# Kernel tuning notes

Hardware: AMD Instinct MI355X
Metric: run time of the kernel (lower is better)

The kernel has to match this reference:

```python
import jax, jax.numpy as jnp
import numpy as np

B, N, S, FIN, H, P = 16, 96, 4, 8, 32, 256  # graphs, nodes, edge feats, node feats, channels, pref pairs


def setup_inputs() -> dict:
    key = jax.random.key(0)
    ks = jax.random.split(key, 12)
    xf = jax.random.normal(ks[0], (B, N, FIN), jnp.float32)
    mask = (jax.random.uniform(ks[1], (B, N, 1)) < 0.9).astype(jnp.float32)
    x = jnp.concatenate([xf, mask], axis=-1)  # last column = node mask (GraphMasking)
    a = (jax.random.uniform(ks[2], (B, N, N)) < 0.1).astype(jnp.float32)  # dense binary adjacency
    e = jax.random.normal(ks[3], (B, N, N, S), jnp.float32)
    pref_a = jax.random.randint(ks[4], (P,), 0, B)
    pref_b = jax.random.randint(ks[5], (P,), 0, B)
    g = lambda k, sh: jax.random.normal(k, sh, jnp.float32) * 0.1
    return dict(
        x=x, a=a, e=e, pref_a=pref_a, pref_b=pref_b,
        W1=g(ks[6], (S, FIN * H)), b1=jnp.zeros((FIN * H,), jnp.float32),
        root1=g(ks[7], (FIN, H)), bias1=jnp.zeros((H,), jnp.float32),
        W2=g(ks[8], (S, H * H)), b2=jnp.zeros((H * H,), jnp.float32),
        root2=g(ks[9], (H, H)), bias2=jnp.zeros((H,), jnp.float32),
        Wd=g(ks[10], (H, 1)), bd=jnp.zeros((1,), jnp.float32),
    )


def ecc_conv(x, a, e, W, b, root, bias, mask, fin, fout):
    # Edge-conditioned filter: Dense(S -> fin*fout) per edge, reshaped [B,N,N,fout,fin]
    K = (e @ W + b).reshape(e.shape[0], e.shape[1], e.shape[2], fout, fin)
    # out[b,n,c] = sum_i a[b,n,i] * sum_f K[b,n,i,c,f] * x[b,i,f]
    out = jnp.einsum("bni,bnicf,bif->bnc", a, K, x)
    out = out + x @ root + bias   # root skip + bias
    out = out * mask              # keras mask propagated from GraphMasking
    return jax.nn.relu(out)


def reference(x, a, e, pref_a, pref_b, W1, b1, root1, bias1, W2, b2, root2, bias2, Wd, bd):
    mask = x[..., -1:]            # GraphMasking: strip mask column
    h = x[..., :-1]
    h = ecc_conv(h, a, e, W1, b1, root1, bias1, mask, FIN, H)
    h = ecc_conv(h, a, e, W2, b2, root2, bias2, mask, H, H)
    pooled = jnp.sum(h, axis=1)                 # GlobalSumPool -> [B, H]
    score = jax.nn.relu(pooled @ Wd + bd)       # Dense(1, relu) -> [B, 1]
    return score[pref_a] - score[pref_b]        # pref_lookup diff -> [P, 1]
```

## Files before the change

### kernel.cpp

```cpp
#include <hip/hip_runtime.h>

namespace {
constexpr int NB   = 16;
constexpr int NN   = 96;
constexpr int NS   = 4;
constexpr int NFIN = 8;
constexpr int NH   = 32;
constexpr int NP   = 256;
constexpr int NPB  = 8;
constexpr int NCHUNK = NN / NPB;

__global__ __launch_bounds__(256) void k1_layer1(
    const float* __restrict__ x, const float* __restrict__ a,
    const float* __restrict__ e, const float* __restrict__ W1,
    const float* __restrict__ b1, const float* __restrict__ root1,
    const float* __restrict__ bias1, float* __restrict__ h1out)
{
  const int bb    = blockIdx.y;
  const int chunk = blockIdx.x;
  const int t     = threadIdx.x;
  const int g     = t >> 5;
  const int lane  = t & 31;
  const int gn    = chunk * NPB + g;

  __shared__ float  xf[NN][NFIN];
  __shared__ float  xmask[NN];
  __shared__ int    idxL[NPB][NN];
  __shared__ float  avalL[NPB][NN];
  __shared__ float  aeL[NPB][NN * NS];
  __shared__ float4 T1s[NPB][8];
  __shared__ float4 U1s[NPB][2];

  for (int j = t; j < NN * 9; j += 256) {
    int node = j / 9, ch = j - node * 9;
    float v = x[(bb * NN + node) * 9 + ch];
    if (ch < NFIN) xf[node][ch] = v; else xmask[node] = v;
  }

  const float* arow = a + (size_t)(bb * NN + gn) * NN;
  const float* erow = e + (size_t)(bb * NN + gn) * NN * NS;
  int base = 0;
  for (int r = 0; r < 3; ++r) {
    int i = r * 32 + lane;
    float av = arow[i];
    unsigned long long bal = __ballot(av != 0.0f);
    unsigned int m = ((t & 63) < 32) ? (unsigned int)bal : (unsigned int)(bal >> 32);
    int pref = __popc(m & ((1u << lane) - 1u));
    if (av != 0.0f) {
      int slot = base + pref;
      idxL[g][slot]  = i;
      avalL[g][slot] = av;
      float4 e4 = *(const float4*)(erow + i * NS);
      aeL[g][slot * 4 + 0] = av * e4.x;
      aeL[g][slot * 4 + 1] = av * e4.y;
      aeL[g][slot * 4 + 2] = av * e4.z;
      aeL[g][slot * 4 + 3] = av * e4.w;
    }
    base += __popc(m);
  }
  const int cnt = base;
  __syncthreads();

  const int s = lane >> 3, f = lane & 7;
  float accT = 0.f, accU = 0.f;
  for (int j = 0; j < cnt; ++j) {
    int   idx = idxL[g][j];
    float av  = avalL[g][j];
    float ae  = aeL[g][j * 4 + s];
    float hv  = xf[idx][f];
    accT = fmaf(ae, hv, accT);
    accU = fmaf(av, hv, accU);
  }
  ((float*)T1s[g])[s * 8 + f] = accT;
  if (s == 0) ((float*)U1s[g])[f] = accU;
  __syncthreads();

  const int c = lane;
  float E = bias1[c];
  const float4* W1_4 = (const float4*)W1;
  for (int ss = 0; ss < 4; ++ss)
    for (int f4 = 0; f4 < 2; ++f4) {
      float4 w  = W1_4[ss * 64 + c * 2 + f4];
      float4 tt = T1s[g][ss * 2 + f4];
      E = fmaf(w.x, tt.x, E); E = fmaf(w.y, tt.y, E);
      E = fmaf(w.z, tt.z, E); E = fmaf(w.w, tt.w, E);
    }
  const float4* b1_4 = (const float4*)b1;
  for (int q = 0; q < 2; ++q) {
    float4 w = b1_4[c * 2 + q];
    float4 u = U1s[g][q];
    E = fmaf(w.x, u.x, E); E = fmaf(w.y, u.y, E);
    E = fmaf(w.z, u.z, E); E = fmaf(w.w, u.w, E);
  }
  for (int ff = 0; ff < NFIN; ++ff)
    E = fmaf(xf[gn][ff], root1[ff * NH + c], E);
  float hv = E * xmask[gn];
  h1out[(size_t)(bb * NN + gn) * NH + c] = hv > 0.f ? hv : 0.f;
}

__global__ __launch_bounds__(256) void k2_layer2(
    const float* __restrict__ x, const float* __restrict__ a,
    const float* __restrict__ e, const float* __restrict__ W2,
    const float* __restrict__ b2, const float* __restrict__ root2,
    const float* __restrict__ bias2, const float* __restrict__ h1,
    float* __restrict__ poolp)
{
  const int bb    = blockIdx.y;
  const int chunk = blockIdx.x;
  const int t     = threadIdx.x;
  const int g     = t >> 5;
  const int lane  = t & 31;
  const int gn    = chunk * NPB + g;

  __shared__ float4 h1s[NN * 8];
  __shared__ int    idxL[NPB][NN];
  __shared__ float  avalL[NPB][NN];
  __shared__ float  aeL[NPB][NN * NS];
  __shared__ float4 T2s[NPB][32];
  __shared__ float4 U2s[NPB][8];
  __shared__ float  h2s[NPB][NH];
  __shared__ float  maskL[NPB];

  const float4* h1v = (const float4*)h1;
  for (int j = t; j < NN * 8; j += 256) h1s[j] = h1v[(size_t)bb * NN * 8 + j];
  if (lane == 0) maskL[g] = x[(size_t)(bb * NN + gn) * 9 + 8];

  const float* arow = a + (size_t)(bb * NN + gn) * NN;
  const float* erow = e + (size_t)(bb * NN + gn) * NN * NS;
  int base = 0;
  for (int r = 0; r < 3; ++r) {
    int i = r * 32 + lane;
    float av = arow[i];
    unsigned long long bal = __ballot(av != 0.0f);
    unsigned int m = ((t & 63) < 32) ? (unsigned int)bal : (unsigned int)(bal >> 32);
    int pref = __popc(m & ((1u << lane) - 1u));
    if (av != 0.0f) {
      int slot = base + pref;
      idxL[g][slot]  = i;
      avalL[g][slot] = av;
      float4 e4 = *(const float4*)(erow + i * NS);
      aeL[g][slot * 4 + 0] = av * e4.x;
      aeL[g][slot * 4 + 1] = av * e4.y;
      aeL[g][slot * 4 + 2] = av * e4.z;
      aeL[g][slot * 4 + 3] = av * e4.w;
    }
    base += __popc(m);
  }
  const int cnt = base;
  __syncthreads();

  const int s = lane >> 3, f4 = lane & 7;
  float4 accT = make_float4(0.f, 0.f, 0.f, 0.f);
  float4 accU = make_float4(0.f, 0.f, 0.f, 0.f);
  for (int j = 0; j < cnt; ++j) {
    int    idx = idxL[g][j];
    float  av  = avalL[g][j];
    float  ae  = aeL[g][j * 4 + s];
    float4 h4  = h1s[idx * 8 + f4];
    accT.x = fmaf(ae, h4.x, accT.x); accT.y = fmaf(ae, h4.y, accT.y);
    accT.z = fmaf(ae, h4.z, accT.z); accT.w = fmaf(ae, h4.w, accT.w);
    accU.x = fmaf(av, h4.x, accU.x); accU.y = fmaf(av, h4.y, accU.y);
    accU.z = fmaf(av, h4.z, accU.z); accU.w = fmaf(av, h4.w, accU.w);
  }
  T2s[g][s * 8 + f4] = accT;
  if (s == 0) U2s[g][f4] = accU;
  __syncthreads();

  const int c = lane;
  float E = bias2[c];
  const float4* W2_4 = (const float4*)W2;
  for (int ss = 0; ss < 4; ++ss)
    for (int q = 0; q < 8; ++q) {
      float4 w  = W2_4[ss * 256 + c * 8 + q];
      float4 tt = T2s[g][ss * 8 + q];
      E = fmaf(w.x, tt.x, E); E = fmaf(w.y, tt.y, E);
      E = fmaf(w.z, tt.z, E); E = fmaf(w.w, tt.w, E);
    }
  const float4* b2_4 = (const float4*)b2;
  for (int q = 0; q < 8; ++q) {
    float4 w = b2_4[c * 8 + q];
    float4 u = U2s[g][q];
    E = fmaf(w.x, u.x, E); E = fmaf(w.y, u.y, E);
    E = fmaf(w.z, u.z, E); E = fmaf(w.w, u.w, E);
  }
  for (int q = 0; q < 8; ++q) {
    float4 hh = h1s[gn * 8 + q];
    E = fmaf(hh.x, root2[(q * 4 + 0) * NH + c], E);
    E = fmaf(hh.y, root2[(q * 4 + 1) * NH + c], E);
    E = fmaf(hh.z, root2[(q * 4 + 2) * NH + c], E);
    E = fmaf(hh.w, root2[(q * 4 + 3) * NH + c], E);
  }
  float hv = E * maskL[g];
  h2s[g][c] = hv > 0.f ? hv : 0.f;
  __syncthreads();

  if (t < NH) {
    float p = 0.f;
    for (int n = 0; n < NPB; ++n) p += h2s[n][t];
    poolp[(size_t)(bb * NCHUNK + chunk) * NH + t] = p;
  }
}

__global__ __launch_bounds__(512) void k3_score(
    const float* __restrict__ poolp, const float* __restrict__ Wd,
    const float* __restrict__ bd, const int* __restrict__ pa,
    const int* __restrict__ pb, float* __restrict__ out)
{
  __shared__ float scores[NB];
  const int t = threadIdx.x;
  const int bb = t >> 5, c = t & 31;
  float v = 0.f;
  for (int k = 0; k < NCHUNK; ++k) v += poolp[(bb * NCHUNK + k) * NH + c];
  v *= Wd[c];
  v += __shfl_xor(v, 16);
  v += __shfl_xor(v, 8);
  v += __shfl_xor(v, 4);
  v += __shfl_xor(v, 2);
  v += __shfl_xor(v, 1);
  if (c == 0) {
    float sc = v + bd[0];
    scores[bb] = sc > 0.f ? sc : 0.f;
  }
  __syncthreads();
  if (t < NP) out[t] = scores[pa[t]] - scores[pb[t]];
}

}

extern "C" void kernel_launch(void* const* d_in, const int* in_sizes, int n_in,
                              void* d_out, int out_size, void* d_ws, size_t ws_size,
                              hipStream_t stream) {
  const float* x     = (const float*)d_in[0];
  const float* a     = (const float*)d_in[1];
  const float* e     = (const float*)d_in[2];
  const int*   pa    = (const int*)d_in[3];
  const int*   pb    = (const int*)d_in[4];
  const float* W1    = (const float*)d_in[5];
  const float* b1    = (const float*)d_in[6];
  const float* root1 = (const float*)d_in[7];
  const float* bias1 = (const float*)d_in[8];
  const float* W2    = (const float*)d_in[9];
  const float* b2    = (const float*)d_in[10];
  const float* root2 = (const float*)d_in[11];
  const float* bias2 = (const float*)d_in[12];
  const float* Wd    = (const float*)d_in[13];
  const float* bd    = (const float*)d_in[14];

  float* h1    = (float*)d_ws;
  float* poolp = h1 + NB * NN * NH;
  float* out   = (float*)d_out;

  dim3 grid(NCHUNK, NB);
  k1_layer1<<<grid, 256, 0, stream>>>(x, a, e, W1, b1, root1, bias1, h1);
  k2_layer2<<<grid, 256, 0, stream>>>(x, a, e, W2, b2, root2, bias2, h1, poolp);
  k3_score<<<1, 512, 0, stream>>>(poolp, Wd, bd, pa, pb, out);
}
```

Baseline: 20.45 us.

## Fuse both ECC layers and pooling into one per-graph kernel

Replaces the three launches (layer 1, layer 2, score) with a single kernel that runs one 1024-thread block per graph, keeps h1 in shared memory, and computes the pooled score in-block. A small gather kernel then forms the preference differences. The neighbour index list is built once and reused by both layers, the adjacency value is treated as binary (multiplication by a dropped), and e is read directly from global memory per neighbour. This removes a launch and the h1 round trip through global memory, at the cost of only 16 blocks on the GPU and each wave handling three nodes in sequence.

```diff
diff --git a/kernel.cpp b/kernel.cpp
--- a/kernel.cpp
+++ b/kernel.cpp
@@ -7,222 +7,179 @@
 constexpr int NFIN = 8;
 constexpr int NH   = 32;
 constexpr int NP   = 256;
-constexpr int NPB  = 8;
-constexpr int NCHUNK = NN / NPB;
-
-__global__ __launch_bounds__(256) void k1_layer1(
+
+__global__ __launch_bounds__(1024) void k_fused(
     const float* __restrict__ x, const float* __restrict__ a,
-    const float* __restrict__ e, const float* __restrict__ W1,
-    const float* __restrict__ b1, const float* __restrict__ root1,
-    const float* __restrict__ bias1, float* __restrict__ h1out)
+    const float* __restrict__ e,
+    const float* __restrict__ W1, const float* __restrict__ b1,
+    const float* __restrict__ root1, const float* __restrict__ bias1,
+    const float* __restrict__ W2, const float* __restrict__ b2,
+    const float* __restrict__ root2, const float* __restrict__ bias2,
+    const float* __restrict__ Wd, const float* __restrict__ bd,
+    float* __restrict__ scores)
 {
-  const int bb    = blockIdx.y;
-  const int chunk = blockIdx.x;
-  const int t     = threadIdx.x;
-  const int g     = t >> 5;
-  const int lane  = t & 31;
-  const int gn    = chunk * NPB + g;
-
-  __shared__ float  xf[NN][NFIN];
-  __shared__ float  xmask[NN];
-  __shared__ int    idxL[NPB][NN];
-  __shared__ float  avalL[NPB][NN];
-  __shared__ float  aeL[NPB][NN * NS];
-  __shared__ float4 T1s[NPB][8];
-  __shared__ float4 U1s[NPB][2];
-
-  for (int j = t; j < NN * 9; j += 256) {
-    int node = j / 9, ch = j - node * 9;
+  const int bb   = blockIdx.x;
+  const int t    = threadIdx.x;
+  const int g    = t >> 5;
+  const int lane = t & 31;
+
+  __shared__ float xf[NN][NFIN];
+  __shared__ float xmask[NN];
+  __shared__ __align__(16) float h1s[NN][NH];
+  __shared__ unsigned char idxc[NN][NN];
+  __shared__ int   cnts[NN];
+  __shared__ float4 Tbuf[32][40];
+  __shared__ float pools[32][NH];
+
+  if (t < NN * 9) {
+    int node = t / 9, ch = t - node * 9;
     float v = x[(bb * NN + node) * 9 + ch];
     if (ch < NFIN) xf[node][ch] = v; else xmask[node] = v;
   }
 
-  const float* arow = a + (size_t)(bb * NN + gn) * NN;
-  const float* erow = e + (size_t)(bb * NN + gn) * NN * NS;
-  int base = 0;
-  for (int r = 0; r < 3; ++r) {
-    int i = r * 32 + lane;
-    float av = arow[i];
-    unsigned long long bal = __ballot(av != 0.0f);
-    unsigned int m = ((t & 63) < 32) ? (unsigned int)bal : (unsigned int)(bal >> 32);
-    int pref = __popc(m & ((1u << lane) - 1u));
-    if (av != 0.0f) {
-      int slot = base + pref;
-      idxL[g][slot]  = i;
-      avalL[g][slot] = av;
-      float4 e4 = *(const float4*)(erow + i * NS);
-      aeL[g][slot * 4 + 0] = av * e4.x;
-      aeL[g][slot * 4 + 1] = av * e4.y;
-      aeL[g][slot * 4 + 2] = av * e4.z;
-      aeL[g][slot * 4 + 3] = av * e4.w;
-    }
-    base += __popc(m);
-  }
-  const int cnt = base;
+  for (int cr = 0; cr < 3; ++cr) {
+    const int n = cr * 32 + g;
+    const float* arow = a + (size_t)(bb * NN + n) * NN;
+    int base = 0;
+    for (int rr = 0; rr < 3; ++rr) {
+      int i = rr * 32 + lane;
+      float av = arow[i];
+      unsigned long long bal = __ballot(av != 0.0f);
+      unsigned int m = ((t & 63) < 32) ? (unsigned int)bal
+                                       : (unsigned int)(bal >> 32);
+      if (av != 0.0f)
+        idxc[n][base + __popc(m & ((1u << lane) - 1u))] = (unsigned char)i;
+      base += __popc(m);
+    }
+    if (lane == 0) cnts[n] = base;
+  }
   __syncthreads();
 
-  const int s = lane >> 3, f = lane & 7;
-  float accT = 0.f, accU = 0.f;
-  for (int j = 0; j < cnt; ++j) {
-    int   idx = idxL[g][j];
-    float av  = avalL[g][j];
-    float ae  = aeL[g][j * 4 + s];
-    float hv  = xf[idx][f];
-    accT = fmaf(ae, hv, accT);
-    accU = fmaf(av, hv, accU);
-  }
-  ((float*)T1s[g])[s * 8 + f] = accT;
-  if (s == 0) ((float*)U1s[g])[f] = accU;
+  {
+    const int s = lane >> 3, f = lane & 7;
+    float* Tb = (float*)&Tbuf[g][0];
+    for (int r = 0; r < 3; ++r) {
+      const int n = r * 32 + g;
+      const int cnt = cnts[n];
+      const float* eb = e + (size_t)(bb * NN + n) * NN * NS + s;
+      float accT = 0.f, accU = 0.f;
+      for (int j = 0; j < cnt; ++j) {
+        int idx = idxc[n][j];
+        float xv = xf[idx][f];
+        accT = fmaf(eb[idx * NS], xv, accT);
+        accU += xv;
+      }
+      Tb[s * 8 + f] = accT;
+      if (s == 0) Tb[128 + f] = accU;
+
+      const int c = lane;
+      float E = bias1[c];
+      const float4* W1_4 = (const float4*)W1;
+      #pragma unroll
+      for (int ss = 0; ss < 4; ++ss)
+        #pragma unroll
+        for (int q = 0; q < 2; ++q) {
+          float4 w  = W1_4[ss * 64 + c * 2 + q];
+          float4 tt = ((const float4*)Tb)[ss * 2 + q];
+          E = fmaf(w.x, tt.x, E); E = fmaf(w.y, tt.y, E);
+          E = fmaf(w.z, tt.z, E); E = fmaf(w.w, tt.w, E);
+        }
+      const float4* b1_4 = (const float4*)b1;
+      #pragma unroll
+      for (int q = 0; q < 2; ++q) {
+        float4 w = b1_4[c * 2 + q];
+        float4 u = ((const float4*)Tb)[32 + q];
+        E = fmaf(w.x, u.x, E); E = fmaf(w.y, u.y, E);
+        E = fmaf(w.z, u.z, E); E = fmaf(w.w, u.w, E);
+      }
+      #pragma unroll
+      for (int ff = 0; ff < NFIN; ++ff)
+        E = fmaf(xf[n][ff], root1[ff * NH + c], E);
+      float hv = E * xmask[n];
+      h1s[n][c] = hv > 0.f ? hv : 0.f;
+    }
+  }
   __syncthreads();
 
-  const int c = lane;
-  float E = bias1[c];
-  const float4* W1_4 = (const float4*)W1;
-  for (int ss = 0; ss < 4; ++ss)
-    for (int f4 = 0; f4 < 2; ++f4) {
-      float4 w  = W1_4[ss * 64 + c * 2 + f4];
-      float4 tt = T1s[g][ss * 2 + f4];
-      E = fmaf(w.x, tt.x, E); E = fmaf(w.y, tt.y, E);
-      E = fmaf(w.z, tt.z, E); E = fmaf(w.w, tt.w, E);
-    }
-  const float4* b1_4 = (const float4*)b1;
-  for (int q = 0; q < 2; ++q) {
-    float4 w = b1_4[c * 2 + q];
-    float4 u = U1s[g][q];
-    E = fmaf(w.x, u.x, E); E = fmaf(w.y, u.y, E);
-    E = fmaf(w.z, u.z, E); E = fmaf(w.w, u.w, E);
-  }
-  for (int ff = 0; ff < NFIN; ++ff)
-    E = fmaf(xf[gn][ff], root1[ff * NH + c], E);
-  float hv = E * xmask[gn];
-  h1out[(size_t)(bb * NN + gn) * NH + c] = hv > 0.f ? hv : 0.f;
-}
-
-__global__ __launch_bounds__(256) void k2_layer2(
-    const float* __restrict__ x, const float* __restrict__ a,
-    const float* __restrict__ e, const float* __restrict__ W2,
-    const float* __restrict__ b2, const float* __restrict__ root2,
-    const float* __restrict__ bias2, const float* __restrict__ h1,
-    float* __restrict__ poolp)
-{
-  const int bb    = blockIdx.y;
-  const int chunk = blockIdx.x;
-  const int t     = threadIdx.x;
-  const int g     = t >> 5;
-  const int lane  = t & 31;
-  const int gn    = chunk * NPB + g;
-
-  __shared__ float4 h1s[NN * 8];
-  __shared__ int    idxL[NPB][NN];
-  __shared__ float  avalL[NPB][NN];
-  __shared__ float  aeL[NPB][NN * NS];
-  __shared__ float4 T2s[NPB][32];
-  __shared__ float4 U2s[NPB][8];
-  __shared__ float  h2s[NPB][NH];
-  __shared__ float  maskL[NPB];
-
-  const float4* h1v = (const float4*)h1;
-  for (int j = t; j < NN * 8; j += 256) h1s[j] = h1v[(size_t)bb * NN * 8 + j];
-  if (lane == 0) maskL[g] = x[(size_t)(bb * NN + gn) * 9 + 8];
-
-  const float* arow = a + (size_t)(bb * NN + gn) * NN;
-  const float* erow = e + (size_t)(bb * NN + gn) * NN * NS;
-  int base = 0;
-  for (int r = 0; r < 3; ++r) {
-    int i = r * 32 + lane;
-    float av = arow[i];
-    unsigned long long bal = __ballot(av != 0.0f);
-    unsigned int m = ((t & 63) < 32) ? (unsigned int)bal : (unsigned int)(bal >> 32);
-    int pref = __popc(m & ((1u << lane) - 1u));
-    if (av != 0.0f) {
-      int slot = base + pref;
-      idxL[g][slot]  = i;
-      avalL[g][slot] = av;
-      float4 e4 = *(const float4*)(erow + i * NS);
-      aeL[g][slot * 4 + 0] = av * e4.x;
-      aeL[g][slot * 4 + 1] = av * e4.y;
-      aeL[g][slot * 4 + 2] = av * e4.z;
-      aeL[g][slot * 4 + 3] = av * e4.w;
-    }
-    base += __popc(m);
-  }
-  const int cnt = base;
+  {
+    const int s = lane >> 3, f4 = lane & 7;
+    float4* T2 = &Tbuf[g][0];
+    float poolacc = 0.f;
+    for (int r = 0; r < 3; ++r) {
+      const int n = r * 32 + g;
+      const int cnt = cnts[n];
+      const float* eb = e + (size_t)(bb * NN + n) * NN * NS + s;
+      float4 accT = make_float4(0.f, 0.f, 0.f, 0.f);
+      float4 accU = make_float4(0.f, 0.f, 0.f, 0.f);
+      for (int j = 0; j < cnt; ++j) {
+        int idx = idxc[n][j];
+        float4 h4 = *(const float4*)&h1s[idx][f4 * 4];
+        float ev = eb[idx * NS];
+        accT.x = fmaf(ev, h4.x, accT.x); accT.y = fmaf(ev, h4.y, accT.y);
+        accT.z = fmaf(ev, h4.z, accT.z); accT.w = fmaf(ev, h4.w, accT.w);
+        accU.x += h4.x; accU.y += h4.y; accU.z += h4.z; accU.w += h4.w;
+      }
+      T2[s * 8 + f4] = accT;
+      if (s == 0) T2[32 + f4] = accU;
+
+      const int c = lane;
+      float E = bias2[c];
+      const float4* W2_4 = (const float4*)W2;
+      #pragma unroll
+      for (int ss = 0; ss < 4; ++ss)
+        #pragma unroll
+        for (int q = 0; q < 8; ++q) {
+          float4 w  = W2_4[ss * 256 + c * 8 + q];
+          float4 tt = T2[ss * 8 + q];
+          E = fmaf(w.x, tt.x, E); E = fmaf(w.y, tt.y, E);
+          E = fmaf(w.z, tt.z, E); E = fmaf(w.w, tt.w, E);
+        }
+      const float4* b2_4 = (const float4*)b2;
+      #pragma unroll
+      for (int q = 0; q < 8; ++q) {
+        float4 w = b2_4[c * 8 + q];
+        float4 u = T2[32 + q];
+        E = fmaf(w.x, u.x, E); E = fmaf(w.y, u.y, E);
+        E = fmaf(w.z, u.z, E); E = fmaf(w.w, u.w, E);
+      }
+      #pragma unroll
+      for (int q = 0; q < 8; ++q) {
+        float4 hh = *(const float4*)&h1s[n][q * 4];
+        E = fmaf(hh.x, root2[(q * 4 + 0) * NH + c], E);
+        E = fmaf(hh.y, root2[(q * 4 + 1) * NH + c], E);
+        E = fmaf(hh.z, root2[(q * 4 + 2) * NH + c], E);
+        E = fmaf(hh.w, root2[(q * 4 + 3) * NH + c], E);
+      }
+      float hv = E * xmask[n];
+      poolacc += (hv > 0.f ? hv : 0.f);
+    }
+    pools[g][lane] = poolacc;
+  }
   __syncthreads();
 
-  const int s = lane >> 3, f4 = lane & 7;
-  float4 accT = make_float4(0.f, 0.f, 0.f, 0.f);
-  float4 accU = make_float4(0.f, 0.f, 0.f, 0.f);
-  for (int j = 0; j < cnt; ++j) {
-    int    idx = idxL[g][j];
-    float  av  = avalL[g][j];
-    float  ae  = aeL[g][j * 4 + s];
-    float4 h4  = h1s[idx * 8 + f4];
-    accT.x = fmaf(ae, h4.x, accT.x); accT.y = fmaf(ae, h4.y, accT.y);
-    accT.z = fmaf(ae, h4.z, accT.z); accT.w = fmaf(ae, h4.w, accT.w);
-    accU.x = fmaf(av, h4.x, accU.x); accU.y = fmaf(av, h4.y, accU.y);
-    accU.z = fmaf(av, h4.z, accU.z); accU.w = fmaf(av, h4.w, accU.w);
-  }
-  T2s[g][s * 8 + f4] = accT;
-  if (s == 0) U2s[g][f4] = accU;
-  __syncthreads();
-
-  const int c = lane;
-  float E = bias2[c];
-  const float4* W2_4 = (const float4*)W2;
-  for (int ss = 0; ss < 4; ++ss)
-    for (int q = 0; q < 8; ++q) {
-      float4 w  = W2_4[ss * 256 + c * 8 + q];
-      float4 tt = T2s[g][ss * 8 + q];
-      E = fmaf(w.x, tt.x, E); E = fmaf(w.y, tt.y, E);
-      E = fmaf(w.z, tt.z, E); E = fmaf(w.w, tt.w, E);
-    }
-  const float4* b2_4 = (const float4*)b2;
-  for (int q = 0; q < 8; ++q) {
-    float4 w = b2_4[c * 8 + q];
-    float4 u = U2s[g][q];
-    E = fmaf(w.x, u.x, E); E = fmaf(w.y, u.y, E);
-    E = fmaf(w.z, u.z, E); E = fmaf(w.w, u.w, E);
-  }
-  for (int q = 0; q < 8; ++q) {
-    float4 hh = h1s[gn * 8 + q];
-    E = fmaf(hh.x, root2[(q * 4 + 0) * NH + c], E);
-    E = fmaf(hh.y, root2[(q * 4 + 1) * NH + c], E);
-    E = fmaf(hh.z, root2[(q * 4 + 2) * NH + c], E);
-    E = fmaf(hh.w, root2[(q * 4 + 3) * NH + c], E);
-  }
-  float hv = E * maskL[g];
-  h2s[g][c] = hv > 0.f ? hv : 0.f;
-  __syncthreads();
-
   if (t < NH) {
-    float p = 0.f;
-    for (int n = 0; n < NPB; ++n) p += h2s[n][t];
-    poolp[(size_t)(bb * NCHUNK + chunk) * NH + t] = p;
-  }
-}
-
-__global__ __launch_bounds__(512) void k3_score(
-    const float* __restrict__ poolp, const float* __restrict__ Wd,
-    const float* __restrict__ bd, const int* __restrict__ pa,
+    float v = 0.f;
+    #pragma unroll
+    for (int gg = 0; gg < 32; ++gg) v += pools[gg][t];
+    v *= Wd[t];
+    v += __shfl_xor(v, 16);
+    v += __shfl_xor(v, 8);
+    v += __shfl_xor(v, 4);
+    v += __shfl_xor(v, 2);
+    v += __shfl_xor(v, 1);
+    if (t == 0) {
+      float sc = v + bd[0];
+      scores[bb] = sc > 0.f ? sc : 0.f;
+    }
+  }
+}
+
+__global__ __launch_bounds__(256) void k_gather(
+    const float* __restrict__ scores, const int* __restrict__ pa,
     const int* __restrict__ pb, float* __restrict__ out)
 {
-  __shared__ float scores[NB];
   const int t = threadIdx.x;
-  const int bb = t >> 5, c = t & 31;
-  float v = 0.f;
-  for (int k = 0; k < NCHUNK; ++k) v += poolp[(bb * NCHUNK + k) * NH + c];
-  v *= Wd[c];
-  v += __shfl_xor(v, 16);
-  v += __shfl_xor(v, 8);
-  v += __shfl_xor(v, 4);
-  v += __shfl_xor(v, 2);
-  v += __shfl_xor(v, 1);
-  if (c == 0) {
-    float sc = v + bd[0];
-    scores[bb] = sc > 0.f ? sc : 0.f;
-  }
-  __syncthreads();
-  if (t < NP) out[t] = scores[pa[t]] - scores[pb[t]];
+  out[t] = scores[pa[t]] - scores[pb[t]];
 }
 
 }
@@ -246,12 +203,10 @@
   const float* Wd    = (const float*)d_in[13];
   const float* bd    = (const float*)d_in[14];
 
-  float* h1    = (float*)d_ws;
-  float* poolp = h1 + NB * NN * NH;
-  float* out   = (float*)d_out;
-
-  dim3 grid(NCHUNK, NB);
-  k1_layer1<<<grid, 256, 0, stream>>>(x, a, e, W1, b1, root1, bias1, h1);
-  k2_layer2<<<grid, 256, 0, stream>>>(x, a, e, W2, b2, root2, bias2, h1, poolp);
-  k3_score<<<1, 512, 0, stream>>>(poolp, Wd, bd, pa, pb, out);
-}
+  float* scores = (float*)d_ws;
+  float* out    = (float*)d_out;
+
+  k_fused<<<NB, 1024, 0, stream>>>(x, a, e, W1, b1, root1, bias1,
+                                   W2, b2, root2, bias2, Wd, bd, scores);
+  k_gather<<<1, NP, 0, stream>>>(scores, pa, pb, out);
+}
```

After: 73.58 us. 3.6x slower.
